# Kernel optimization log

Hardware: AMD Instinct MI355X
Metric: run time of the kernel (lower is better)

## Reference

```python
import jax, jax.numpy as jnp
import numpy as np

B, S, D = 8, 1024, 1024
H, K = 16, 64  # num_heads, key_dim
NEG_INF = -1e9  # Keras _large_compatible_negative for float32


def setup_inputs() -> dict:
    key = jax.random.key(0)
    ks = jax.random.split(key, 10)
    x = jax.random.normal(ks[0], (B, S, D), dtype=jnp.float32)
    mask = jax.random.bernoulli(ks[1], 0.9, (B, S))  # bool per-token mask
    w = lambda k, shp: (0.02 * jax.random.normal(k, shp, dtype=jnp.float32))
    return {
        "input_tensor": x,
        "input_mask": mask,
        "Wq": w(ks[2], (D, H, K)), "bq": jnp.zeros((H, K), jnp.float32),
        "Wk": w(ks[3], (D, H, K)), "bk": jnp.zeros((H, K), jnp.float32),
        "Wv": w(ks[4], (D, H, K)), "bv": jnp.zeros((H, K), jnp.float32),
        "Wo": w(ks[5], (H, K, D)), "bo": jnp.zeros((D,), jnp.float32),
    }


def reference(input_tensor, input_mask, Wq, bq, Wk, bk, Wv, bv, Wo, bo):
    x = input_tensor
    # QKV projections: [B,S,D] x [D,H,K] -> [B,S,H,K]
    q = jnp.einsum("bsd,dhk->bshk", x, Wq) + bq
    k = jnp.einsum("bsd,dhk->bshk", x, Wk) + bk
    v = jnp.einsum("bsd,dhk->bshk", x, Wv) + bv
    # scaled dot-product scores: [B,H,Sq,Sk]
    scores = jnp.einsum("bqhk,bshk->bhqs", q, k) / jnp.sqrt(
        jnp.asarray(K, x.dtype))
    # mask = logical_and(mask[...,None], mask[...,None,:]) per example
    m2 = (input_mask[:, :, None] & input_mask[:, None, :])  # [B,Sq,Sk]
    scores = scores + (1.0 - m2[:, None, :, :].astype(x.dtype)) * NEG_INF
    probs = jax.nn.softmax(scores, axis=-1)
    # attend and project out: [B,S,H,K] -> [B,S,D]
    ctx = jnp.einsum("bhqs,bshk->bqhk", probs, v)
    return jnp.einsum("bqhk,hkd->bqd", ctx, Wo) + bo
```

## Files before the change

kernel.cpp:

```cpp
#include <hip/hip_runtime.h>
#include <math.h>

#define Ss 1024
#define Dd 1024
#define Hh 16
#define Kk 64

typedef __bf16 bf16x8 __attribute__((ext_vector_type(8)));
typedef __bf16 bf16x4 __attribute__((ext_vector_type(4)));
typedef float  f32x4  __attribute__((ext_vector_type(4)));

#define MFMA16(a, b, c) __builtin_amdgcn_mfma_f32_16x16x32_bf16(a, b, c, 0, 0, 0)

#define XB_E   8388608u
#define WT_E   3145728u
#define WOT_E  1048576u
#define QKV_E  8388608u

__global__ __launch_bounds__(256) void prep(
    const float* __restrict__ x,
    const float* __restrict__ Wq, const float* __restrict__ Wk,
    const float* __restrict__ Wv, const float* __restrict__ Wo,
    __bf16* __restrict__ xb, __bf16* __restrict__ WT, __bf16* __restrict__ WoT)
{
    __shared__ float tile[64][65];
    const int z = blockIdx.z;
    const int t = threadIdx.x;

    if (z == 4) {
        size_t blk = blockIdx.y * 16 + blockIdx.x;
        const float4* src = (const float4*)(x + blk * 32768);
        bf16x4* dst = (bf16x4*)(((__bf16*)xb) + blk * 32768);
        #pragma unroll
        for (int u = 0; u < 32; ++u) {
            float4 v = src[u * 256 + t];
            dst[u * 256 + t] =
                (bf16x4){(__bf16)v.x, (__bf16)v.y, (__bf16)v.z, (__bf16)v.w};
        }
        return;
    }

    const float* src = (z == 0) ? Wq : (z == 1) ? Wk : (z == 2) ? Wv : Wo;
    __bf16* dst = (z < 3) ? (WT + (size_t)z * 1048576) : WoT;

    int r0 = blockIdx.y * 64, c0 = blockIdx.x * 64;
    int rr = t >> 2, cg = (t & 3) * 16;

    #pragma unroll
    for (int u = 0; u < 4; ++u) {
        float4 v = *(const float4*)(src + (size_t)(r0 + rr) * 1024 + c0 + cg + u * 4);
        tile[rr][cg + u * 4 + 0] = v.x;
        tile[rr][cg + u * 4 + 1] = v.y;
        tile[rr][cg + u * 4 + 2] = v.z;
        tile[rr][cg + u * 4 + 3] = v.w;
    }
    __syncthreads();
    bf16x8 o0, o1;
    #pragma unroll
    for (int jj = 0; jj < 8; ++jj) o0[jj] = (__bf16)tile[cg + jj][rr];
    #pragma unroll
    for (int jj = 0; jj < 8; ++jj) o1[jj] = (__bf16)tile[cg + 8 + jj][rr];
    __bf16* dp = dst + (size_t)(c0 + rr) * 1024 + r0 + cg;
    *(bf16x8*)dp = o0;
    *(bf16x8*)(dp + 8) = o1;
}

__global__ __launch_bounds__(256) void gemm_bt(
    const __bf16* __restrict__ A, const __bf16* __restrict__ Bt, int mode,
    __bf16* __restrict__ qb, __bf16* __restrict__ kb, __bf16* __restrict__ vb,
    const float* __restrict__ bq, const float* __restrict__ bk,
    const float* __restrict__ bv,
    float* __restrict__ outf, const float* __restrict__ bo)
{
    __shared__ __align__(16) __bf16 As[2][128][32];
    __shared__ __align__(16) __bf16 Bs[2][128][32];

    const int t = threadIdx.x;
    const int wave = t >> 6, lane = t & 63;
    const int quad = lane >> 4, l16 = lane & 15;
    const int wm = wave >> 1, wn = wave & 1;
    const int m0 = blockIdx.y * 128, n0 = blockIdx.x * 128;

    const int sr = t >> 2;
    const int sc = (t & 3) * 8;

    f32x4 acc[4][4];
    #pragma unroll
    for (int i = 0; i < 4; ++i)
        #pragma unroll
        for (int j = 0; j < 4; ++j) acc[i][j] = (f32x4){0.f, 0.f, 0.f, 0.f};

    const __bf16* pa0 = A + (size_t)(m0 + sr) * 1024 + sc;
    const __bf16* pa1 = A + (size_t)(m0 + sr + 64) * 1024 + sc;
    const __bf16* pb0 = Bt + (size_t)(n0 + sr) * 1024 + sc;
    const __bf16* pb1 = Bt + (size_t)(n0 + sr + 64) * 1024 + sc;

    bf16x8 ra0 = *(const bf16x8*)(pa0);
    bf16x8 ra1 = *(const bf16x8*)(pa1);
    bf16x8 rb0 = *(const bf16x8*)(pb0);
    bf16x8 rb1 = *(const bf16x8*)(pb1);

    for (int k0 = 0; k0 < 1024; k0 += 32) {
        const int p = (k0 >> 5) & 1;
        *(bf16x8*)&As[p][sr][sc] = ra0;
        *(bf16x8*)&As[p][sr + 64][sc] = ra1;
        *(bf16x8*)&Bs[p][sr][sc] = rb0;
        *(bf16x8*)&Bs[p][sr + 64][sc] = rb1;
        __syncthreads();

        const int kn = k0 + 32;
        if (kn < 1024) {
            ra0 = *(const bf16x8*)(pa0 + kn);
            ra1 = *(const bf16x8*)(pa1 + kn);
            rb0 = *(const bf16x8*)(pb0 + kn);
            rb1 = *(const bf16x8*)(pb1 + kn);
        }

        bf16x8 af[4], bfr[4];
        #pragma unroll
        for (int i = 0; i < 4; ++i)
            af[i] = *(const bf16x8*)&As[p][wm * 64 + i * 16 + l16][quad * 8];
        #pragma unroll
        for (int j = 0; j < 4; ++j)
            bfr[j] = *(const bf16x8*)&Bs[p][wn * 64 + j * 16 + l16][quad * 8];
        #pragma unroll
        for (int i = 0; i < 4; ++i)
            #pragma unroll
            for (int j = 0; j < 4; ++j)
                acc[i][j] = MFMA16(af[i], bfr[j], acc[i][j]);
    }

    if (mode == 0) {
        const int z = n0 >> 10;
        const float* bias = (z == 0) ? bq : (z == 1) ? bk : bv;
        const float sc2 = (z == 0) ? 0.125f : 1.0f;
        #pragma unroll
        for (int i = 0; i < 4; ++i) {
            int row = m0 + wm * 64 + i * 16 + quad * 4;
            int b = row >> 10, s = row & 1023;
            #pragma unroll
            for (int j = 0; j < 4; ++j) {
                int n1 = (n0 + wn * 64 + j * 16 + l16) & 1023;
                int h = n1 >> 6, ch = n1 & 63;
                float bia = bias[n1];
                if (z < 2) {
                    __bf16* dst = ((z == 0) ? qb : kb)
                        + ((size_t)(b * Hh + h) * Ss + s) * Kk + ch;
                    #pragma unroll
                    for (int r = 0; r < 4; ++r)
                        dst[(size_t)r * Kk] = (__bf16)((acc[i][j][r] + bia) * sc2);
                } else {
                    bf16x4 o;
                    #pragma unroll
                    for (int r = 0; r < 4; ++r) o[r] = (__bf16)(acc[i][j][r] + bia);
                    *(bf16x4*)(vb + ((size_t)(b * Hh + h) * Kk + ch) * Ss + s) = o;
                }
            }
        }
    } else {
        #pragma unroll
        for (int i = 0; i < 4; ++i) {
            int row = m0 + wm * 64 + i * 16 + quad * 4;
            #pragma unroll
            for (int j = 0; j < 4; ++j) {
                int n = n0 + wn * 64 + j * 16 + l16;
                float bia = bo[n];
                #pragma unroll
                for (int r = 0; r < 4; ++r)
                    outf[(size_t)(row + r) * 1024 + n] = acc[i][j][r] + bia;
            }
        }
    }
}

__global__ __launch_bounds__(256) void attn(
    const __bf16* __restrict__ qb, const __bf16* __restrict__ kb,
    const __bf16* __restrict__ vb, const int* __restrict__ mask,
    __bf16* __restrict__ ctx)
{
    const int bh = blockIdx.x;
    const int q0 = blockIdx.y * 128;
    const int b  = bh >> 4;
    const int h  = bh & 15;
    const size_t base = (size_t)bh * Ss * Kk;

    __shared__ __align__(16) __bf16 Qs[128][72];
    __shared__ __align__(16) __bf16 Ks[64][72];
    __shared__ __align__(16) __bf16 VTs[64][72];
    __shared__ __align__(16) __bf16 Ps[4][32][72];
    __shared__ float mkf[1024];

    const int t    = threadIdx.x;
    const int wave = t >> 6, lane = t & 63;
    const int quad = lane >> 4, l16 = lane & 15;
    const int qbase = wave * 32;

    #pragma unroll
    for (int p = 0; p < 4; ++p) {
        int idx = t + p * 256;
        int r = idx >> 3, g = idx & 7;
        *(bf16x8*)&Qs[r][g * 8] =
            *(const bf16x8*)(qb + base + (size_t)(q0 + r) * Kk + g * 8);
    }
    {
        int4 mi = *(const int4*)(mask + b * Ss + t * 4);
        mkf[t * 4 + 0] = (float)mi.x;
        mkf[t * 4 + 1] = (float)mi.y;
        mkf[t * 4 + 2] = (float)mi.z;
        mkf[t * 4 + 3] = (float)mi.w;
    }

    const int r0 = t >> 3, c0 = (t & 7) * 8;
    bf16x8 kr0, kr1, vr0, vr1;
    kr0 = *(const bf16x8*)(kb + base + (size_t)(r0) * Kk + c0);
    kr1 = *(const bf16x8*)(kb + base + (size_t)(r0 + 32) * Kk + c0);
    vr0 = *(const bf16x8*)(vb + base + (size_t)(r0) * Ss + c0);
    vr1 = *(const bf16x8*)(vb + base + (size_t)(r0 + 32) * Ss + c0);

    __syncthreads();

    bf16x8 aq[2][2];
    #pragma unroll
    for (int rg = 0; rg < 2; ++rg) {
        aq[rg][0] = *(const bf16x8*)&Qs[qbase + rg * 16 + l16][quad * 8];
        aq[rg][1] = *(const bf16x8*)&Qs[qbase + rg * 16 + l16][32 + quad * 8];
    }
    float mqf[2][4], omqf[2][4];
    #pragma unroll
    for (int rg = 0; rg < 2; ++rg)
        #pragma unroll
        for (int i = 0; i < 4; ++i) {
            float m = mkf[q0 + qbase + rg * 16 + quad * 4 + i];
            mqf[rg][i] = m; omqf[rg][i] = 1.0f - m;
        }

    f32x4 O[2][4];
    float lsum[2][4];
    #pragma unroll
    for (int rg = 0; rg < 2; ++rg)
        #pragma unroll
        for (int nb = 0; nb < 4; ++nb) O[rg][nb] = (f32x4){0.f, 0.f, 0.f, 0.f};
    #pragma unroll
    for (int rg = 0; rg < 2; ++rg)
        #pragma unroll
        for (int i = 0; i < 4; ++i) lsum[rg][i] = 0.f;

    for (int kt = 0; kt < Ss; kt += 64) {
        __syncthreads();
        *(bf16x8*)&Ks[r0][c0] = kr0;
        *(bf16x8*)&Ks[r0 + 32][c0] = kr1;
        *(bf16x8*)&VTs[r0][c0] = vr0;
        *(bf16x8*)&VTs[r0 + 32][c0] = vr1;
        __syncthreads();

        int ktn = kt + 64;
        if (ktn < Ss) {
            kr0 = *(const bf16x8*)(kb + base + (size_t)(ktn + r0) * Kk + c0);
            kr1 = *(const bf16x8*)(kb + base + (size_t)(ktn + r0 + 32) * Kk + c0);
            vr0 = *(const bf16x8*)(vb + base + (size_t)(r0) * Ss + ktn + c0);
            vr1 = *(const bf16x8*)(vb + base + (size_t)(r0 + 32) * Ss + ktn + c0);
        }

        float mkv[4];
        #pragma unroll
        for (int nb = 0; nb < 4; ++nb) mkv[nb] = mkf[kt + nb * 16 + l16];

        bf16x8 kb0[4], kb1[4];
        #pragma unroll
        for (int nb = 0; nb < 4; ++nb) {
            kb0[nb] = *(const bf16x8*)&Ks[nb * 16 + l16][quad * 8];
            kb1[nb] = *(const bf16x8*)&Ks[nb * 16 + l16][32 + quad * 8];
        }

        f32x4 s[2][4];
        #pragma unroll
        for (int rg = 0; rg < 2; ++rg)
            #pragma unroll
            for (int nb = 0; nb < 4; ++nb) {
                f32x4 a = (f32x4){0.f, 0.f, 0.f, 0.f};
                a = MFMA16(aq[rg][0], kb0[nb], a);
                a = MFMA16(aq[rg][1], kb1[nb], a);
                s[rg][nb] = a;
            }

        #pragma unroll
        for (int rg = 0; rg < 2; ++rg)
            #pragma unroll
            for (int i = 0; i < 4; ++i) {
                float ls = 0.f;
                #pragma unroll
                for (int nb = 0; nb < 4; ++nb) {
                    float p = __expf(s[rg][nb][i]) * mkv[nb];
                    p = p * mqf[rg][i] + omqf[rg][i];
                    Ps[wave][rg * 16 + quad * 4 + i][nb * 16 + l16] = (__bf16)p;
                    ls += p;
                }
                lsum[rg][i] += ls;
            }

        bf16x8 ap0[2], ap1[2];
        #pragma unroll
        for (int rg = 0; rg < 2; ++rg) {
            ap0[rg] = *(const bf16x8*)&Ps[wave][rg * 16 + l16][quad * 8];
            ap1[rg] = *(const bf16x8*)&Ps[wave][rg * 16 + l16][32 + quad * 8];
        }
        #pragma unroll
        for (int nb = 0; nb < 4; ++nb) {
            bf16x8 vb0 = *(const bf16x8*)&VTs[nb * 16 + l16][quad * 8];
            bf16x8 vb1 = *(const bf16x8*)&VTs[nb * 16 + l16][32 + quad * 8];
            #pragma unroll
            for (int rg = 0; rg < 2; ++rg) {
                O[rg][nb] = MFMA16(ap0[rg], vb0, O[rg][nb]);
                O[rg][nb] = MFMA16(ap1[rg], vb1, O[rg][nb]);
            }
        }
    }

    #pragma unroll
    for (int rg = 0; rg < 2; ++rg)
        #pragma unroll
        for (int i = 0; i < 4; ++i) {
            float l = lsum[rg][i];
            l += __shfl_xor(l, 1);
            l += __shfl_xor(l, 2);
            l += __shfl_xor(l, 4);
            l += __shfl_xor(l, 8);
            float inv = 1.0f / l;
            int srow = q0 + qbase + rg * 16 + quad * 4 + i;
            __bf16* dst = ctx + ((size_t)(b * Ss + srow) * Hh + h) * Kk;
            #pragma unroll
            for (int nb = 0; nb < 4; ++nb)
                dst[nb * 16 + l16] = (__bf16)(O[rg][nb][i] * inv);
        }
}

extern "C" void kernel_launch(void* const* d_in, const int* in_sizes, int n_in,
                              void* d_out, int out_size, void* d_ws, size_t ws_size,
                              hipStream_t stream) {
    const float* x    = (const float*)d_in[0];
    const int*   mask = (const int*)d_in[1];
    const float* Wq   = (const float*)d_in[2];
    const float* bq   = (const float*)d_in[3];
    const float* Wk   = (const float*)d_in[4];
    const float* bk   = (const float*)d_in[5];
    const float* Wv   = (const float*)d_in[6];
    const float* bv   = (const float*)d_in[7];
    const float* Wo   = (const float*)d_in[8];
    const float* bo   = (const float*)d_in[9];

    __bf16* xb   = (__bf16*)d_ws;
    __bf16* WT   = xb + XB_E;
    __bf16* WoT  = WT + WT_E;
    __bf16* qb   = WoT + WOT_E;
    __bf16* kb   = qb + QKV_E;
    __bf16* vb   = kb + QKV_E;
    __bf16* ctxb = vb + QKV_E;
    float* out = (float*)d_out;

    prep<<<dim3(16, 16, 5), 256, 0, stream>>>(x, Wq, Wk, Wv, Wo, xb, WT, WoT);
    gemm_bt<<<dim3(24, 64), 256, 0, stream>>>(xb, WT, 0, qb, kb, vb,
                                              bq, bk, bv, nullptr, nullptr);
    attn<<<dim3(128, 8), 256, 0, stream>>>(qb, kb, vb, mask, ctxb);
    gemm_bt<<<dim3(8, 64), 256, 0, stream>>>(ctxb, WoT, 1, nullptr, nullptr,
                                             nullptr, nullptr, nullptr, nullptr,
                                             out, bo);
}
```

Measured before the change: 273.5 us.

## Double-buffer K/V tiles, fold log2e into Q scale, use hardware exp2, set MFMA priority

The K and V shared-memory tiles in the attention kernel are double-buffered, which removes one __syncthreads per key tile. The Q projection scale now includes log2(e), so the softmax can call the raw v_exp_f32 instruction in place of __expf. The MFMA blocks are wrapped in s_setprio so matrix work gets issue priority over other waves. Risks: with a single barrier per iteration, reuse of a buffer two iterations later relies on ordering that is still believed to hold. The hardware exp2 may also lose a little precision.

```diff
diff --git a/kernel.cpp b/kernel.cpp
--- a/kernel.cpp
+++ b/kernel.cpp
@@ -16,6 +16,10 @@
 #define WT_E   3145728u
 #define WOT_E  1048576u
 #define QKV_E  8388608u
+
+__device__ __forceinline__ float exp2_hw(float x) {
+    float r; asm("v_exp_f32 %0, %1" : "=v"(r) : "v"(x)); return r;
+}
 
 __global__ __launch_bounds__(256) void prep(
     const float* __restrict__ x,
@@ -133,7 +137,7 @@
     if (mode == 0) {
         const int z = n0 >> 10;
         const float* bias = (z == 0) ? bq : (z == 1) ? bk : bv;
-        const float sc2 = (z == 0) ? 0.125f : 1.0f;
+        const float sc2 = (z == 0) ? 0.18033688011112042f : 1.0f;
         #pragma unroll
         for (int i = 0; i < 4; ++i) {
             int row = m0 + wm * 64 + i * 16 + quad * 4;
@@ -185,8 +189,8 @@
     const size_t base = (size_t)bh * Ss * Kk;
 
     __shared__ __align__(16) __bf16 Qs[128][72];
-    __shared__ __align__(16) __bf16 Ks[64][72];
-    __shared__ __align__(16) __bf16 VTs[64][72];
+    __shared__ __align__(16) __bf16 Ks[2][64][72];
+    __shared__ __align__(16) __bf16 VTs[2][64][72];
     __shared__ __align__(16) __bf16 Ps[4][32][72];
     __shared__ float mkf[1024];
 
@@ -246,11 +250,11 @@
         for (int i = 0; i < 4; ++i) lsum[rg][i] = 0.f;
 
     for (int kt = 0; kt < Ss; kt += 64) {
-        __syncthreads();
-        *(bf16x8*)&Ks[r0][c0] = kr0;
-        *(bf16x8*)&Ks[r0 + 32][c0] = kr1;
-        *(bf16x8*)&VTs[r0][c0] = vr0;
-        *(bf16x8*)&VTs[r0 + 32][c0] = vr1;
+        const int p = (kt >> 6) & 1;
+        *(bf16x8*)&Ks[p][r0][c0] = kr0;
+        *(bf16x8*)&Ks[p][r0 + 32][c0] = kr1;
+        *(bf16x8*)&VTs[p][r0][c0] = vr0;
+        *(bf16x8*)&VTs[p][r0 + 32][c0] = vr1;
         __syncthreads();
 
         int ktn = kt + 64;
@@ -268,11 +272,12 @@
         bf16x8 kb0[4], kb1[4];
         #pragma unroll
         for (int nb = 0; nb < 4; ++nb) {
-            kb0[nb] = *(const bf16x8*)&Ks[nb * 16 + l16][quad * 8];
-            kb1[nb] = *(const bf16x8*)&Ks[nb * 16 + l16][32 + quad * 8];
+            kb0[nb] = *(const bf16x8*)&Ks[p][nb * 16 + l16][quad * 8];
+            kb1[nb] = *(const bf16x8*)&Ks[p][nb * 16 + l16][32 + quad * 8];
         }
 
         f32x4 s[2][4];
+        __builtin_amdgcn_s_setprio(1);
         #pragma unroll
         for (int rg = 0; rg < 2; ++rg)
             #pragma unroll
@@ -282,6 +287,7 @@
                 a = MFMA16(aq[rg][1], kb1[nb], a);
                 s[rg][nb] = a;
             }
+        __builtin_amdgcn_s_setprio(0);
 
         #pragma unroll
         for (int rg = 0; rg < 2; ++rg)
@@ -290,10 +296,10 @@
                 float ls = 0.f;
                 #pragma unroll
                 for (int nb = 0; nb < 4; ++nb) {
-                    float p = __expf(s[rg][nb][i]) * mkv[nb];
-                    p = p * mqf[rg][i] + omqf[rg][i];
-                    Ps[wave][rg * 16 + quad * 4 + i][nb * 16 + l16] = (__bf16)p;
-                    ls += p;
+                    float pv = exp2_hw(s[rg][nb][i]) * mkv[nb];
+                    pv = pv * mqf[rg][i] + omqf[rg][i];
+                    Ps[wave][rg * 16 + quad * 4 + i][nb * 16 + l16] = (__bf16)pv;
+                    ls += pv;
                 }
                 lsum[rg][i] += ls;
             }
@@ -304,16 +310,18 @@
             ap0[rg] = *(const bf16x8*)&Ps[wave][rg * 16 + l16][quad * 8];
             ap1[rg] = *(const bf16x8*)&Ps[wave][rg * 16 + l16][32 + quad * 8];
         }
+        __builtin_amdgcn_s_setprio(1);
         #pragma unroll
         for (int nb = 0; nb < 4; ++nb) {
-            bf16x8 vb0 = *(const bf16x8*)&VTs[nb * 16 + l16][quad * 8];
-            bf16x8 vb1 = *(const bf16x8*)&VTs[nb * 16 + l16][32 + quad * 8];
+            bf16x8 vb0 = *(const bf16x8*)&VTs[p][nb * 16 + l16][quad * 8];
+            bf16x8 vb1 = *(const bf16x8*)&VTs[p][nb * 16 + l16][32 + quad * 8];
             #pragma unroll
             for (int rg = 0; rg < 2; ++rg) {
                 O[rg][nb] = MFMA16(ap0[rg], vb0, O[rg][nb]);
                 O[rg][nb] = MFMA16(ap1[rg], vb1, O[rg][nb]);
             }
         }
+        __builtin_amdgcn_s_setprio(0);
     }
 
     #pragma unroll
```

Measured after the change: 271.7 us. No clear change (-0.7%).
